# Kernel optimization log

Hardware: AMD Instinct MI355X
Metric: run time of the kernel (lower is better)

Reference implementation:

```python
import jax, jax.numpy as jnp
import numpy as np

B, S, F, H, P = 2048, 168, 7, 128, 96  # batch, window, features, hidden, pred_len


def setup_inputs() -> dict:
    key = jax.random.key(0)
    ks = jax.random.split(key, 16)
    sc = 0.05
    return {
        "xb": jax.random.normal(ks[0], (B, S, F), dtype=jnp.float32),
        # encoder LSTM (1 layer, unidirectional); gate order i,f,g,o like torch
        "W_ih_enc": jax.random.normal(ks[1], (4 * H, F), dtype=jnp.float32) * sc,
        "W_hh_enc": jax.random.normal(ks[2], (4 * H, H), dtype=jnp.float32) * sc,
        "b_ih_enc": jax.random.normal(ks[3], (4 * H,), dtype=jnp.float32) * sc,
        "b_hh_enc": jax.random.normal(ks[4], (4 * H,), dtype=jnp.float32) * sc,
        # attention linear: (H+F) -> S
        "W_att": jax.random.normal(ks[5], (S, H + F), dtype=jnp.float32) * sc,
        "b_att": jax.random.normal(ks[6], (S,), dtype=jnp.float32) * sc,
        # decoder LSTMCell: input_size=H, hidden=H
        "W_ih_dec": jax.random.normal(ks[7], (4 * H, H), dtype=jnp.float32) * sc,
        "W_hh_dec": jax.random.normal(ks[8], (4 * H, H), dtype=jnp.float32) * sc,
        "b_ih_dec": jax.random.normal(ks[9], (4 * H,), dtype=jnp.float32) * sc,
        "b_hh_dec": jax.random.normal(ks[10], (4 * H,), dtype=jnp.float32) * sc,
        # out linear: H -> F
        "W_out": jax.random.normal(ks[11], (F, H), dtype=jnp.float32) * sc,
        "b_out": jax.random.normal(ks[12], (F,), dtype=jnp.float32) * sc,
        # final linear (output_size==1 branch): F -> 1
        "W_fin": jax.random.normal(ks[13], (1, F), dtype=jnp.float32) * sc,
        "b_fin": jax.random.normal(ks[14], (1,), dtype=jnp.float32) * sc,
    }


def _gates(pre):
    i, f, g, o = jnp.split(pre, 4, axis=-1)
    return jax.nn.sigmoid(i), jax.nn.sigmoid(f), jnp.tanh(g), jax.nn.sigmoid(o)


def _forward(xb, W_ih_enc, W_hh_enc, b_ih_enc, b_hh_enc, W_att, b_att,
             W_ih_dec, W_hh_dec, b_ih_dec, b_hh_dec, W_out, b_out, W_fin, b_fin):
    b_enc = b_ih_enc + b_hh_enc
    x_ih = jnp.einsum('bsf,gf->sbg', xb, W_ih_enc)  # precompute input projections [S,B,4H]

    def enc_step(carry, xg):
        h, c = carry
        i, f, g, o = _gates(xg + h @ W_hh_enc.T + b_enc)
        c = f * c + i * g
        h = o * jnp.tanh(c)
        return (h, c), h

    h0 = jnp.zeros((xb.shape[0], W_hh_enc.shape[1]), dtype=xb.dtype)
    (h_T, _), enc_hs = jax.lax.scan(enc_step, (h0, h0), x_ih)
    encoder_output = jnp.transpose(enc_hs, (1, 0, 2))  # [B,S,H]

    b_dec = b_ih_dec + b_hh_dec

    def dec_step(carry, _):
        prev_h, y_prev = carry
        attn_in = jnp.concatenate([prev_h, y_prev], axis=1)          # [B,H+F]
        attn_w = jax.nn.softmax(attn_in @ W_att.T + b_att, axis=-1)  # [B,S]
        combine = jnp.einsum('bs,bsh->bh', attn_w, encoder_output)   # [B,H]
        # torch code: rnn_hidden, rnn_hidden = cell(combine, (prev_h, prev_h))
        # -> the CELL state c' is what survives; h'/output gate discarded.
        i, f, g, _ = _gates(combine @ W_ih_dec.T + prev_h @ W_hh_dec.T + b_dec)
        c_new = f * prev_h + i * g
        out = c_new @ W_out.T + b_out                                # [B,F]
        return (c_new, out), out

    y0 = xb[:, -1, :]
    _, outs = jax.lax.scan(dec_step, (h_T, y0), None, length=P)      # [P,B,F]
    outputs = jnp.transpose(outs, (1, 0, 2))                         # [B,P,F]
    return outputs @ W_fin.T + b_fin                                 # [B,P,1]


def reference(xb, W_ih_enc, W_hh_enc, b_ih_enc, b_hh_enc, W_att, b_att,
              W_ih_dec, W_hh_dec, b_ih_dec, b_hh_dec, W_out, b_out, W_fin, b_fin):
    return _forward(xb, W_ih_enc, W_hh_enc, b_ih_enc, b_hh_enc, W_att, b_att,
                    W_ih_dec, W_hh_dec, b_ih_dec, b_hh_dec, W_out, b_out, W_fin, b_fin)
```

## Files before the change

kernel.cpp:

```cpp
#include <hip/hip_runtime.h>
#include <hip/hip_fp8.h>

#define NB   2048
#define SEQ  168
#define NF   7
#define NH   128
#define NP   96
#define EROWS 8
#define DROWS 8
#define NTHR 512
#define KE   160
#define KD   256
#define HXS  168
#define CTS  264
#define LS4  30

typedef _Float16 h16;
typedef _Float16 h16x8 __attribute__((ext_vector_type(8)));
typedef float    f32x2 __attribute__((ext_vector_type(2)));
typedef float    f32x4 __attribute__((ext_vector_type(4)));
typedef unsigned int u32x4 __attribute__((ext_vector_type(4)));

__device__ __forceinline__ void mfma_av(f32x4& acc, h16x8 a, const h16x8& b_agpr) {
  asm("v_mfma_f32_16x16x32_f16 %0, %1, %2, %0"
      : "+v"(acc) : "v"(a), "a"(b_agpr));
}
#define PIN_A(x) asm volatile("" : "+a"(x))

__device__ __forceinline__ float sigm(float x) { return 1.f / (1.f + __expf(-x)); }
__device__ __forceinline__ float tanh_(float x) {
  float e = __expf(-2.f * fabsf(x));
  return copysignf((1.f - e) / (1.f + e), x);
}

template <bool HI>
__device__ __forceinline__ unsigned int pack2_fp8(float a, float b, unsigned int old) {
#if __has_builtin(__builtin_amdgcn_cvt_pk_fp8_f32)
  return (unsigned int)__builtin_amdgcn_cvt_pk_fp8_f32(a, b, (int)old, HI);
#else
  __hip_fp8_e4m3 qa(a), qb(b);
  unsigned int pair = (unsigned int)(*(unsigned char*)&qa) |
                      ((unsigned int)(*(unsigned char*)&qb) << 8);
  return HI ? ((old & 0x0000ffffu) | (pair << 16)) : ((old & 0xffff0000u) | pair);
#endif
}
template <bool HI>
__device__ __forceinline__ f32x2 unp2(unsigned int w) {
#if __has_builtin(__builtin_amdgcn_cvt_pk_f32_fp8)
  return __builtin_amdgcn_cvt_pk_f32_fp8(w, HI);
#else
  __hip_fp8_e4m3 a, b;
  constexpr unsigned int sh = HI ? 16 : 0;
  *(unsigned char*)&a = (w >> sh) & 0xff;
  *(unsigned char*)&b = (w >> (sh + 8)) & 0xff;
  f32x2 r; r.x = (float)a; r.y = (float)b; return r;
#endif
}

constexpr size_t WENC_OFF   = 0;
constexpr size_t WDEC_OFF   = 163840;
constexpr size_t WEFF_OFF   = 425984;
constexpr size_t BEFF_OFF   = 468992;
constexpr size_t WCOMB_OFF  = 469760;
constexpr size_t BCONST_OFF = 470272;
constexpr size_t BENC_OFF   = 470528;
constexpr size_t BDEC_OFF   = 472576;
constexpr size_t ENC2_OFF   = 31981568;
constexpr size_t HT_OFF     = 44564480;

constexpr int HIST_OFF   = 0;
constexpr int CATH_OFF   = 122880;
constexpr int ATTW_OFF   = 131328;
constexpr int WAT2_OFF   = 136704;
constexpr int D0_OFF     = 146944;
constexpr int OUTP_OFF   = 152320;
constexpr int YH_OFF     = 152576;
constexpr int DPART_OFF  = 152832;
constexpr int DPART2_OFF = 153088;
constexpr int OBUF_OFF   = 153216;
constexpr int DSMEM      = 153472;
constexpr int SHHX_OFF = 122880;
constexpr int X16_OFF  = 133632;

__global__ void setup_weights(const float* __restrict__ Wih_enc, const float* __restrict__ Whh_enc,
                              const float* __restrict__ Wih_dec, const float* __restrict__ Whh_dec,
                              const float* __restrict__ Watt, const float* __restrict__ batt,
                              const float* __restrict__ Wout, const float* __restrict__ bout,
                              const float* __restrict__ Wfin, const float* __restrict__ bfin,
                              const float* __restrict__ bihe, const float* __restrict__ bhhe,
                              const float* __restrict__ bihd, const float* __restrict__ bhhd,
                              char* __restrict__ ws) {
  int idx = blockIdx.x * blockDim.x + threadIdx.x;
  constexpr int A0 = 81920;
  constexpr int A1 = A0 + 131072;
  constexpr int A2 = A1 + 21504;
  constexpr int A3 = A2 + 168;
  constexpr int A4 = A3 + 128;
  constexpr int A5 = A4 + 1;
  constexpr int A6 = A5 + 512;
  if (idx < A0) {
    int n = idx / KE, k = idx % KE;
    float v = 0.f;
    if (k < NF) v = Wih_enc[n * NF + k];
    else if (k >= 8 && k < 136) v = Whh_enc[n * NH + (k - 8)];
    ((h16*)(ws + WENC_OFF))[idx] = (h16)v;
  } else if (idx < A1) {
    int i = idx - A0;
    int n = i / KD, k = i % KD;
    float v = (k < NH) ? Wih_dec[n * NH + k] : Whh_dec[n * NH + (k - NH)];
    ((h16*)(ws + WDEC_OFF))[i] = (h16)v;
  } else if (idx < A2) {
    int i = idx - A1;
    int s = i / NH, k = i % NH;
    float v = Watt[s * (NH + NF) + k];
    #pragma unroll
    for (int f = 0; f < NF; ++f)
      v += Watt[s * (NH + NF) + NH + f] * Wout[f * NH + k];
    ((h16*)(ws + WEFF_OFF))[i] = (h16)v;
  } else if (idx < A3) {
    int s = idx - A2;
    float v = batt[s];
    #pragma unroll
    for (int f = 0; f < NF; ++f)
      v += Watt[s * (NH + NF) + NH + f] * bout[f];
    ((float*)(ws + BEFF_OFF))[s] = v;
  } else if (idx < A4) {
    int k = idx - A3;
    float v = 0.f;
    #pragma unroll
    for (int f = 0; f < NF; ++f) v += Wfin[f] * Wout[f * NH + k];
    ((float*)(ws + WCOMB_OFF))[k] = v;
  } else if (idx < A5) {
    float v = bfin[0];
    #pragma unroll
    for (int f = 0; f < NF; ++f) v += bout[f] * Wfin[f];
    ((float*)(ws + BCONST_OFF))[0] = v;
  } else if (idx < A6) {
    int g = idx - A5;
    ((float*)(ws + BENC_OFF))[g] = bihe[g] + bhhe[g];
    ((float*)(ws + BDEC_OFF))[g] = bihd[g] + bhhd[g];
  }
}

__global__ __attribute__((amdgpu_flat_work_group_size(NTHR, NTHR), amdgpu_waves_per_eu(2, 2)))
void fused_kernel(const float* __restrict__ xb, const h16* __restrict__ w16enc,
                  const float* __restrict__ bencp, unsigned int* __restrict__ encw2,
                  float* __restrict__ hTg,
                  const float* __restrict__ Watt, const float* __restrict__ Wout,
                  const float* __restrict__ bout,
                  const h16* __restrict__ w16dec, const h16* __restrict__ weff,
                  const float* __restrict__ beffp, const float* __restrict__ wcombp,
                  const float* __restrict__ bconstp, const float* __restrict__ bdecp,
                  float* __restrict__ out) {
  extern __shared__ char smem[];
  unsigned int* hist = (unsigned int*)(smem + HIST_OFF);
  h16 (*sh_hx)[16][HXS] = (h16(*)[16][HXS])(smem + SHHX_OFF);
  h16*   x16      = (h16*)(smem + X16_OFF);
  h16*   sh_cath  = (h16*)(smem + CATH_OFF);
  float* sh_attw  = (float*)(smem + ATTW_OFF);
  h16*   sh_watt2 = (h16*)(smem + WAT2_OFF);
  float* sh_d0    = (float*)(smem + D0_OFF);
  float* sh_outp  = (float*)(smem + OUTP_OFF);
  float* sh_yh    = (float*)(smem + YH_OFF);
  float* sh_dp    = (float*)(smem + DPART_OFF);
  float* sh_dp2   = (float*)(smem + DPART2_OFF);
  float* sh_obuf  = (float*)(smem + OBUF_OFF);

  const int t  = threadIdx.x;
  const int r0 = blockIdx.x * EROWS;

  const int w  = t >> 6;
  const int l  = t & 63;
  const int lq = l >> 4;
  const int ln = l & 15;
  const int hcol = w * 16 + ln;
  const int mrow = lq * 4;
  const bool act = (lq < 2);

  for (int i = t; i < 2 * 16 * HXS; i += NTHR) ((h16*)sh_hx)[i] = (h16)0.f;
  for (int i = t; i < EROWS * SEQ * NF; i += NTHR)
    x16[i] = (h16)xb[(size_t)r0 * SEQ * NF + i];

  h16x8 bfE[4][5];
  float bE[4];
  #pragma unroll
  for (int g = 0; g < 4; ++g) {
    int n = g * 128 + hcol;
    bE[g] = bencp[n];
    #pragma unroll
    for (int kt = 0; kt < 5; ++kt) {
      bfE[g][kt] = *(const h16x8*)(w16enc + n * KE + kt * 32 + lq * 8);
      PIN_A(bfE[g][kt]);
    }
  }
  __syncthreads();
  if (t < EROWS * NF) {
    int r = t / NF, f = t - (t / NF) * NF;
    sh_hx[0][r][f] = x16[(r * SEQ + 0) * NF + f];
  }

  float creg[4] = {0.f, 0.f, 0.f, 0.f};
  float hstate[4] = {0.f, 0.f, 0.f, 0.f};
  float hprev[4] = {0.f, 0.f, 0.f, 0.f};
  unsigned int hpack[4] = {0u, 0u, 0u, 0u};

  __syncthreads();

  for (int s = 0; s < SEQ; ++s) {
    const int cur = s & 1;

    f32x4 ac[4] = {{0.f,0.f,0.f,0.f},{0.f,0.f,0.f,0.f},{0.f,0.f,0.f,0.f},{0.f,0.f,0.f,0.f}};
    #pragma unroll
    for (int kt = 0; kt < 5; ++kt) {
      h16x8 af = *(const h16x8*)(&sh_hx[cur][ln][kt * 32 + lq * 8]);
      #pragma unroll
      for (int g = 0; g < 4; ++g)
        mfma_av(ac[g], af, bfE[g][kt]);
    }

    if (act) {
      #pragma unroll
      for (int reg = 0; reg < 4; ++reg) {
        float gi = sigm(ac[0][reg] + bE[0]);
        float gf = sigm(ac[1][reg] + bE[1]);
        float gg = tanh_(ac[2][reg] + bE[2]);
        float go = sigm(ac[3][reg] + bE[3]);
        float c = gf * creg[reg] + gi * gg;
        creg[reg] = c;
        float h = go * tanh_(c);
        hstate[reg] = h;
        sh_hx[cur ^ 1][mrow + reg][8 + hcol] = (h16)h;
        float hs = h * 16.f;
        if ((s & 1) == 0) hprev[reg] = hs;
        else if ((s & 3) == 1) hpack[reg] = pack2_fp8<false>(hprev[reg], hs, hpack[reg]);
        else                   hpack[reg] = pack2_fp8<true>(hprev[reg], hs, hpack[reg]);
      }
      if ((s & 3) == 3) {
        int s4 = s >> 2;
        if (s4 < LS4) {
          #pragma unroll
          for (int reg = 0; reg < 4; ++reg)
            hist[(size_t)(mrow + reg) * (LS4 * NH) + s4 * NH + hcol] = hpack[reg];
        } else {
          int q = s4 - LS4;
          #pragma unroll
          for (int reg = 0; reg < 4; ++reg)
            encw2[(((size_t)(r0 + mrow + reg) * 3 + (q >> 2)) * NH + hcol) * 4 + (q & 3)] = hpack[reg];
        }
      }
    }
    if (t < EROWS * NF && s + 1 < SEQ) {
      int r = t / NF, f = t - (t / NF) * NF;
      sh_hx[cur ^ 1][r][f] = x16[(r * SEQ + (s + 1)) * NF + f];
    }
    __syncthreads();
  }

  if (act) {
    #pragma unroll
    for (int reg = 0; reg < 4; ++reg)
      hTg[(size_t)(r0 + mrow + reg) * NH + hcol] = hstate[reg];
  }
  __builtin_amdgcn_sched_barrier(0);
  __syncthreads();

  for (int i = t; i < 40 * NH; i += NTHR) sh_watt2[i] = weff[128 * NH + i];
  if (t < 32) sh_dp2[t] = 0.f;

  h16x8 bfD[3][8];
  float bD[3];
  #pragma unroll
  for (int g = 0; g < 3; ++g) {
    int n = g * 128 + hcol;
    bD[g] = bdecp[n];
    #pragma unroll
    for (int kt = 0; kt < 8; ++kt) {
      bfD[g][kt] = *(const h16x8*)(w16dec + n * KD + kt * 32 + lq * 8);
      PIN_A(bfD[g][kt]);
    }
  }
  h16x8 bfA[4];
  #pragma unroll
  for (int kt = 0; kt < 4; ++kt) {
    bfA[kt] = *(const h16x8*)(weff + hcol * NH + kt * 32 + lq * 8);
    PIN_A(bfA[kt]);
  }
  const float beffR = beffp[hcol];
  const int s2v = 128 + hcol;
  const float beff2 = (w < 3 && s2v < SEQ) ? beffp[s2v] : 0.f;
  const float wcombR = wcombp[hcol];
  const float bconstv = bconstp[0];

  if (act) {
    #pragma unroll
    for (int reg = 0; reg < 4; ++reg) {
      creg[reg] = hstate[reg];
      sh_cath[0 * 8 * CTS + (mrow + reg) * CTS + 128 + hcol] = (h16)hstate[reg];
    }
  }
  if (t < DROWS * NF) {
    int r = t / NF, f = t - (t / NF) * NF;
    float a = bout[f];
    const float* wr = Wout + f * NH;
    const float* hp = hTg + (size_t)(r0 + r) * NH;
    #pragma unroll 8
    for (int k = 0; k < NH; k += 4) {
      float4 pv = *(const float4*)(hp + k);
      float4 wv = *(const float4*)(wr + k);
      a += pv.x * wv.x + pv.y * wv.y + pv.z * wv.z + pv.w * wv.w;
    }
    sh_yh[t] = a;
  }
  __syncthreads();
  for (int i = t; i < DROWS * SEQ; i += NTHR) {
    int r = i / SEQ, s = i - (i / SEQ) * SEQ;
    float a = 0.f;
    #pragma unroll
    for (int f = 0; f < NF; ++f) {
      float y0f = xb[((size_t)(r0 + r) * SEQ + (SEQ - 1)) * NF + f];
      a += (y0f - sh_yh[r * NF + f]) * Watt[s * (NH + NF) + NH + f];
    }
    sh_d0[i] = a;
  }

  const int dr = t >> 7;
  const int dh = t & 127;
  const unsigned int* hrowA = hist + (size_t)dr * (LS4 * NH) + dh;
  const unsigned int* hrowB = hist + (size_t)(dr + 4) * (LS4 * NH) + dh;
  const float* erowA = sh_attw + dr * SEQ;
  const float* erowB = sh_attw + (dr + 4) * SEQ;

  u32x4 tA[3], tB[3];
  {
    const u32x4* e2 = (const u32x4*)encw2;
    #pragma unroll
    for (int b = 0; b < 3; ++b) {
      tA[b] = e2[((size_t)(r0 + dr)     * 3 + b) * NH + dh];
      tB[b] = e2[((size_t)(r0 + dr + 4) * 3 + b) * NH + dh];
    }
  }
  __syncthreads();

  f32x4 aghh[3];

  for (int p = 0; p < NP; ++p) {
    const int CA = p & 1;

    if (p > 0 && t < DROWS) {
      float a = bconstv;
      #pragma unroll
      for (int w2 = 0; w2 < 8; ++w2) a += sh_outp[w2 * 8 + t];
      int slot = (p - 1) & 7;
      sh_obuf[t * 8 + slot] = a;
      if (slot == 7) {
        int base = p - 8;
        #pragma unroll
        for (int j = 0; j < 8; ++j)
          out[(size_t)(r0 + t) * NP + base + j] = sh_obuf[t * 8 + j];
      }
    }

    {
      h16x8 afA[4];
      #pragma unroll
      for (int kt = 0; kt < 4; ++kt)
        afA[kt] = *(const h16x8*)(sh_cath + CA * 8 * CTS + (ln & 7) * CTS + 128 + kt * 32 + lq * 8);
      f32x4 acc = {0.f, 0.f, 0.f, 0.f};
      #pragma unroll
      for (int kt = 0; kt < 4; ++kt)
        mfma_av(acc, afA[kt], bfA[kt]);
      #pragma unroll
      for (int g = 0; g < 3; ++g) {
        f32x4 z = {0.f, 0.f, 0.f, 0.f};
        aghh[g] = z;
        #pragma unroll
        for (int kt = 0; kt < 4; ++kt)
          mfma_av(aghh[g], afA[kt], bfD[g][4 + kt]);
      }

      float ev[4];
      if (act) {
        #pragma unroll
        for (int reg = 0; reg < 4; ++reg) {
          int row = mrow + reg;
          float lg = acc[reg] + beffR;
          if (p == 0) lg += sh_d0[row * SEQ + hcol];
          lg = fminf(fmaxf(lg, -30.f), 30.f);
          ev[reg] = __expf(lg);
          sh_attw[row * SEQ + hcol] = ev[reg];
        }
        #pragma unroll
        for (int reg = 0; reg < 4; ++reg) {
          float rs = ev[reg];
          rs += __shfl_xor(rs, 1);
          rs += __shfl_xor(rs, 2);
          rs += __shfl_xor(rs, 4);
          rs += __shfl_xor(rs, 8);
          if (ln == 0) sh_dp[(mrow + reg) * 8 + w] = rs;
        }
      }
      if (w < 3) {
        int srow = (s2v < SEQ ? s2v : SEQ - 1) - 128;
        f32x4 acc2 = {0.f, 0.f, 0.f, 0.f};
        #pragma unroll
        for (int kt = 0; kt < 4; ++kt) {
          h16x8 bf2 = *(const h16x8*)(sh_watt2 + srow * NH + kt * 32 + lq * 8);
          acc2 = __builtin_amdgcn_mfma_f32_16x16x32_f16(afA[kt], bf2, acc2, 0, 0, 0);
        }
        if (act) {
          float ev2[4];
          #pragma unroll
          for (int reg = 0; reg < 4; ++reg) {
            int row = mrow + reg;
            float e2v = 0.f;
            if (s2v < SEQ) {
              float lg = acc2[reg] + beff2;
              if (p == 0) lg += sh_d0[row * SEQ + s2v];
              lg = fminf(fmaxf(lg, -30.f), 30.f);
              e2v = __expf(lg);
              sh_attw[row * SEQ + s2v] = e2v;
            }
            ev2[reg] = e2v;
          }
          #pragma unroll
          for (int reg = 0; reg < 4; ++reg) {
            float rs = ev2[reg];
            rs += __shfl_xor(rs, 1);
            rs += __shfl_xor(rs, 2);
            rs += __shfl_xor(rs, 4);
            rs += __shfl_xor(rs, 8);
            if (ln == 0) sh_dp2[(mrow + reg) * 4 + w] = rs;
          }
        }
      }
    }
    __syncthreads();

    {
      float4 qa0 = *(const float4*)(sh_dp + dr * 8);
      float4 qa1 = *(const float4*)(sh_dp + dr * 8 + 4);
      float4 qa2 = *(const float4*)(sh_dp2 + dr * 4);
      float4 qb0 = *(const float4*)(sh_dp + (dr + 4) * 8);
      float4 qb1 = *(const float4*)(sh_dp + (dr + 4) * 8 + 4);
      float4 qb2 = *(const float4*)(sh_dp2 + (dr + 4) * 4);
      float dA = ((qa0.x + qa0.y) + (qa0.z + qa0.w)) + ((qa1.x + qa1.y) + (qa1.z + qa1.w))
               + ((qa2.x + qa2.y) + (qa2.z + qa2.w));
      float dB = ((qb0.x + qb0.y) + (qb0.z + qb0.w)) + ((qb1.x + qb1.y) + (qb1.z + qb1.w))
               + ((qb2.x + qb2.y) + (qb2.z + qb2.w));
      const float invA = 0.0625f / dA;
      const float invB = 0.0625f / dB;

      f32x2 avA = {0.f, 0.f};
      f32x2 avB = {0.f, 0.f};
      #pragma unroll 6
      for (int s4 = 0; s4 < LS4; ++s4) {
        unsigned int evA = hrowA[s4 * NH];
        unsigned int evB = hrowB[s4 * NH];
        float4 eA = *(const float4*)(erowA + s4 * 4);
        float4 eB = *(const float4*)(erowB + s4 * 4);
        f32x2 wA01 = {eA.x, eA.y}, wA23 = {eA.z, eA.w};
        f32x2 wB01 = {eB.x, eB.y}, wB23 = {eB.z, eB.w};
        avA = wA01 * unp2<false>(evA) + avA;
        avA = wA23 * unp2<true>(evA) + avA;
        avB = wB01 * unp2<false>(evB) + avB;
        avB = wB23 * unp2<true>(evB) + avB;
      }
      #pragma unroll
      for (int b = 0; b < 3; ++b) {
        #pragma unroll
        for (int jj = 0; jj < 4; ++jj) {
          int s4 = LS4 + b * 4 + jj;
          unsigned int evA = tA[b][jj];
          unsigned int evB = tB[b][jj];
          float4 eA = *(const float4*)(erowA + s4 * 4);
          float4 eB = *(const float4*)(erowB + s4 * 4);
          f32x2 wA01 = {eA.x, eA.y}, wA23 = {eA.z, eA.w};
          f32x2 wB01 = {eB.x, eB.y}, wB23 = {eB.z, eB.w};
          avA = wA01 * unp2<false>(evA) + avA;
          avA = wA23 * unp2<true>(evA) + avA;
          avB = wB01 * unp2<false>(evB) + avB;
          avB = wB23 * unp2<true>(evB) + avB;
        }
      }
      sh_cath[CA * 8 * CTS + dr * CTS + dh]       = (h16)((avA.x + avA.y) * invA);
      sh_cath[CA * 8 * CTS + (dr + 4) * CTS + dh] = (h16)((avB.x + avB.y) * invB);
    }
    __syncthreads();

    {
      f32x4 ag[3] = {aghh[0], aghh[1], aghh[2]};
      #pragma unroll
      for (int kt = 0; kt < 4; ++kt) {
        h16x8 af = *(const h16x8*)(sh_cath + CA * 8 * CTS + (ln & 7) * CTS + kt * 32 + lq * 8);
        #pragma unroll
        for (int g = 0; g < 3; ++g)
          mfma_av(ag[g], af, bfD[g][kt]);
      }
      if (act) {
        float contrib[4];
        #pragma unroll
        for (int reg = 0; reg < 4; ++reg) {
          int row = mrow + reg;
          float gi = sigm(ag[0][reg] + bD[0]);
          float gf = sigm(ag[1][reg] + bD[1]);
          float gg = tanh_(ag[2][reg] + bD[2]);
          float cn = gf * creg[reg] + gi * gg;
          creg[reg] = cn;
          sh_cath[(CA ^ 1) * 8 * CTS + row * CTS + 128 + hcol] = (h16)cn;
          contrib[reg] = cn * wcombR;
        }
        #pragma unroll
        for (int reg = 0; reg < 4; ++reg) {
          float rsum = contrib[reg];
          rsum += __shfl_xor(rsum, 1);
          rsum += __shfl_xor(rsum, 2);
          rsum += __shfl_xor(rsum, 4);
          rsum += __shfl_xor(rsum, 8);
          if (ln == 0) sh_outp[w * 8 + mrow + reg] = rsum;
        }
      }
    }
    __syncthreads();
  }

  if (t < DROWS) {
    float a = bconstv;
    #pragma unroll
    for (int w2 = 0; w2 < 8; ++w2) a += sh_outp[w2 * 8 + t];
    sh_obuf[t * 8 + 7] = a;
    #pragma unroll
    for (int j = 0; j < 8; ++j)
      out[(size_t)(r0 + t) * NP + (NP - 8) + j] = sh_obuf[t * 8 + j];
  }
}

extern "C" void kernel_launch(void* const* d_in, const int* in_sizes, int n_in,
                              void* d_out, int out_size, void* d_ws, size_t ws_size,
                              hipStream_t stream) {
  const float* xb      = (const float*)d_in[0];
  const float* Wih_enc = (const float*)d_in[1];
  const float* Whh_enc = (const float*)d_in[2];
  const float* bih_enc = (const float*)d_in[3];
  const float* bhh_enc = (const float*)d_in[4];
  const float* Watt    = (const float*)d_in[5];
  const float* batt    = (const float*)d_in[6];
  const float* Wih_dec = (const float*)d_in[7];
  const float* Whh_dec = (const float*)d_in[8];
  const float* bih_dec = (const float*)d_in[9];
  const float* bhh_dec = (const float*)d_in[10];
  const float* Wout    = (const float*)d_in[11];
  const float* bout    = (const float*)d_in[12];
  const float* Wfin    = (const float*)d_in[13];
  const float* bfin    = (const float*)d_in[14];
  char* ws = (char*)d_ws;

  hipFuncSetAttribute(reinterpret_cast<const void*>(fused_kernel),
                      hipFuncAttributeMaxDynamicSharedMemorySize, DSMEM);

  setup_weights<<<920, 256, 0, stream>>>(Wih_enc, Whh_enc, Wih_dec, Whh_dec,
                                         Watt, batt, Wout, bout, Wfin, bfin,
                                         bih_enc, bhh_enc, bih_dec, bhh_dec, ws);
  fused_kernel<<<NB / EROWS, NTHR, DSMEM, stream>>>(
      xb, (const h16*)(ws + WENC_OFF), (const float*)(ws + BENC_OFF),
      (unsigned int*)(ws + ENC2_OFF), (float*)(ws + HT_OFF),
      Watt, Wout, bout,
      (const h16*)(ws + WDEC_OFF), (const h16*)(ws + WEFF_OFF),
      (const float*)(ws + BEFF_OFF), (const float*)(ws + WCOMB_OFF),
      (const float*)(ws + BCONST_OFF), (const float*)(ws + BDEC_OFF),
      (float*)d_out);
}
```

Baseline: 996.0 us.

## Stream encoder inputs from global, recompute softmax denominators, drop early hidden MFMAs

The encoder no longer stages the whole x window in LDS. Each group of threads prefetches four future timesteps into a register every fourth step and writes them into the shared input tile. In the decoder, the softmax denominator is now recomputed by a full-wave shuffle reduction over the stored exponentials instead of per-warp partial sums kept in shared memory. The hidden-state gate MFMAs are moved back into the post-attention gate loop (8 k-tiles instead of 4), which shortens the attention phase but lengthens the gate phase and adds global loads inside the recurrent loop.

```diff
diff --git a/kernel.cpp b/kernel.cpp
--- a/kernel.cpp
+++ b/kernel.cpp
@@ -75,12 +75,9 @@
 constexpr int D0_OFF     = 146944;
 constexpr int OUTP_OFF   = 152320;
 constexpr int YH_OFF     = 152576;
-constexpr int DPART_OFF  = 152832;
-constexpr int DPART2_OFF = 153088;
-constexpr int OBUF_OFF   = 153216;
-constexpr int DSMEM      = 153472;
+constexpr int OBUF_OFF   = 152832;
+constexpr int DSMEM      = 153088;
 constexpr int SHHX_OFF = 122880;
-constexpr int X16_OFF  = 133632;
 
 __global__ void setup_weights(const float* __restrict__ Wih_enc, const float* __restrict__ Whh_enc,
                               const float* __restrict__ Wih_dec, const float* __restrict__ Whh_dec,
@@ -155,15 +152,12 @@
   extern __shared__ char smem[];
   unsigned int* hist = (unsigned int*)(smem + HIST_OFF);
   h16 (*sh_hx)[16][HXS] = (h16(*)[16][HXS])(smem + SHHX_OFF);
-  h16*   x16      = (h16*)(smem + X16_OFF);
   h16*   sh_cath  = (h16*)(smem + CATH_OFF);
   float* sh_attw  = (float*)(smem + ATTW_OFF);
   h16*   sh_watt2 = (h16*)(smem + WAT2_OFF);
   float* sh_d0    = (float*)(smem + D0_OFF);
   float* sh_outp  = (float*)(smem + OUTP_OFF);
   float* sh_yh    = (float*)(smem + YH_OFF);
-  float* sh_dp    = (float*)(smem + DPART_OFF);
-  float* sh_dp2   = (float*)(smem + DPART2_OFF);
   float* sh_obuf  = (float*)(smem + OBUF_OFF);
 
   const int t  = threadIdx.x;
@@ -177,9 +171,12 @@
   const int mrow = lq * 4;
   const bool act = (lq < 2);
 
+  const int j  = t & 3;
+  const int rf = t >> 2;
+  const int xr = rf / NF;
+  const int xf = rf - xr * NF;
+
   for (int i = t; i < 2 * 16 * HXS; i += NTHR) ((h16*)sh_hx)[i] = (h16)0.f;
-  for (int i = t; i < EROWS * SEQ * NF; i += NTHR)
-    x16[i] = (h16)xb[(size_t)r0 * SEQ * NF + i];
 
   h16x8 bfE[4][5];
   float bE[4];
@@ -196,18 +193,23 @@
   __syncthreads();
   if (t < EROWS * NF) {
     int r = t / NF, f = t - (t / NF) * NF;
-    sh_hx[0][r][f] = x16[(r * SEQ + 0) * NF + f];
+    sh_hx[0][r][f] = (h16)xb[((size_t)(r0 + r) * SEQ + 0) * NF + f];
   }
 
   float creg[4] = {0.f, 0.f, 0.f, 0.f};
   float hstate[4] = {0.f, 0.f, 0.f, 0.f};
   float hprev[4] = {0.f, 0.f, 0.f, 0.f};
   unsigned int hpack[4] = {0u, 0u, 0u, 0u};
+  float xstash = 0.f;
 
   __syncthreads();
 
   for (int s = 0; s < SEQ; ++s) {
     const int cur = s & 1;
+    if ((s & 3) == 0 && t < EROWS * NF * 4) {
+      int sx = s + 1 + j;
+      xstash = (sx < SEQ) ? xb[((size_t)(r0 + xr) * SEQ + sx) * NF + xf] : 0.f;
+    }
 
     f32x4 ac[4] = {{0.f,0.f,0.f,0.f},{0.f,0.f,0.f,0.f},{0.f,0.f,0.f,0.f},{0.f,0.f,0.f,0.f}};
     #pragma unroll
@@ -249,10 +251,8 @@
         }
       }
     }
-    if (t < EROWS * NF && s + 1 < SEQ) {
-      int r = t / NF, f = t - (t / NF) * NF;
-      sh_hx[cur ^ 1][r][f] = x16[(r * SEQ + (s + 1)) * NF + f];
-    }
+    if (t < EROWS * NF * 4 && (s & 3) == j && s + 1 < SEQ)
+      sh_hx[cur ^ 1][xr][xf] = (h16)xstash;
     __syncthreads();
   }
 
@@ -261,11 +261,9 @@
     for (int reg = 0; reg < 4; ++reg)
       hTg[(size_t)(r0 + mrow + reg) * NH + hcol] = hstate[reg];
   }
-  __builtin_amdgcn_sched_barrier(0);
   __syncthreads();
 
   for (int i = t; i < 40 * NH; i += NTHR) sh_watt2[i] = weff[128 * NH + i];
-  if (t < 32) sh_dp2[t] = 0.f;
 
   h16x8 bfD[3][8];
   float bD[3];
@@ -341,8 +339,6 @@
   }
   __syncthreads();
 
-  f32x4 aghh[3];
-
   for (int p = 0; p < NP; ++p) {
     const int CA = p & 1;
 
@@ -355,8 +351,8 @@
       if (slot == 7) {
         int base = p - 8;
         #pragma unroll
-        for (int j = 0; j < 8; ++j)
-          out[(size_t)(r0 + t) * NP + base + j] = sh_obuf[t * 8 + j];
+        for (int jj = 0; jj < 8; ++jj)
+          out[(size_t)(r0 + t) * NP + base + jj] = sh_obuf[t * 8 + jj];
       }
     }
 
@@ -369,16 +365,6 @@
       #pragma unroll
       for (int kt = 0; kt < 4; ++kt)
         mfma_av(acc, afA[kt], bfA[kt]);
-      #pragma unroll
-      for (int g = 0; g < 3; ++g) {
-        f32x4 z = {0.f, 0.f, 0.f, 0.f};
-        aghh[g] = z;
-        #pragma unroll
-        for (int kt = 0; kt < 4; ++kt)
-          mfma_av(aghh[g], afA[kt], bfD[g][4 + kt]);
-      }
-
-      float ev[4];
       if (act) {
         #pragma unroll
         for (int reg = 0; reg < 4; ++reg) {
@@ -386,17 +372,7 @@
           float lg = acc[reg] + beffR;
           if (p == 0) lg += sh_d0[row * SEQ + hcol];
           lg = fminf(fmaxf(lg, -30.f), 30.f);
-          ev[reg] = __expf(lg);
-          sh_attw[row * SEQ + hcol] = ev[reg];
-        }
-        #pragma unroll
-        for (int reg = 0; reg < 4; ++reg) {
-          float rs = ev[reg];
-          rs += __shfl_xor(rs, 1);
-          rs += __shfl_xor(rs, 2);
-          rs += __shfl_xor(rs, 4);
-          rs += __shfl_xor(rs, 8);
-          if (ln == 0) sh_dp[(mrow + reg) * 8 + w] = rs;
+          sh_attw[row * SEQ + hcol] = __expf(lg);
         }
       }
       if (w < 3) {
@@ -407,46 +383,29 @@
           h16x8 bf2 = *(const h16x8*)(sh_watt2 + srow * NH + kt * 32 + lq * 8);
           acc2 = __builtin_amdgcn_mfma_f32_16x16x32_f16(afA[kt], bf2, acc2, 0, 0, 0);
         }
-        if (act) {
-          float ev2[4];
+        if (s2v < SEQ && act) {
           #pragma unroll
           for (int reg = 0; reg < 4; ++reg) {
             int row = mrow + reg;
-            float e2v = 0.f;
-            if (s2v < SEQ) {
-              float lg = acc2[reg] + beff2;
-              if (p == 0) lg += sh_d0[row * SEQ + s2v];
-              lg = fminf(fmaxf(lg, -30.f), 30.f);
-              e2v = __expf(lg);
-              sh_attw[row * SEQ + s2v] = e2v;
-            }
-            ev2[reg] = e2v;
+            float lg = acc2[reg] + beff2;
+            if (p == 0) lg += sh_d0[row * SEQ + s2v];
+            lg = fminf(fmaxf(lg, -30.f), 30.f);
+            sh_attw[row * SEQ + s2v] = __expf(lg);
           }
-          #pragma unroll
-          for (int reg = 0; reg < 4; ++reg) {
-            float rs = ev2[reg];
-            rs += __shfl_xor(rs, 1);
-            rs += __shfl_xor(rs, 2);
-            rs += __shfl_xor(rs, 4);
-            rs += __shfl_xor(rs, 8);
-            if (ln == 0) sh_dp2[(mrow + reg) * 4 + w] = rs;
-          }
         }
       }
     }
     __syncthreads();
 
     {
-      float4 qa0 = *(const float4*)(sh_dp + dr * 8);
-      float4 qa1 = *(const float4*)(sh_dp + dr * 8 + 4);
-      float4 qa2 = *(const float4*)(sh_dp2 + dr * 4);
-      float4 qb0 = *(const float4*)(sh_dp + (dr + 4) * 8);
-      float4 qb1 = *(const float4*)(sh_dp + (dr + 4) * 8 + 4);
-      float4 qb2 = *(const float4*)(sh_dp2 + (dr + 4) * 4);
-      float dA = ((qa0.x + qa0.y) + (qa0.z + qa0.w)) + ((qa1.x + qa1.y) + (qa1.z + qa1.w))
-               + ((qa2.x + qa2.y) + (qa2.z + qa2.w));
-      float dB = ((qb0.x + qb0.y) + (qb0.z + qb0.w)) + ((qb1.x + qb1.y) + (qb1.z + qb1.w))
-               + ((qb2.x + qb2.y) + (qb2.z + qb2.w));
+      float dA = erowA[l] + erowA[64 + l];
+      float dB = erowB[l] + erowB[64 + l];
+      if (l < SEQ - 128) { dA += erowA[128 + l]; dB += erowB[128 + l]; }
+      #pragma unroll
+      for (int k = 1; k < 64; k <<= 1) {
+        dA += __shfl_xor(dA, k);
+        dB += __shfl_xor(dB, k);
+      }
       const float invA = 0.0625f / dA;
       const float invB = 0.0625f / dB;
 
@@ -488,9 +447,9 @@
     __syncthreads();
 
     {
-      f32x4 ag[3] = {aghh[0], aghh[1], aghh[2]};
-      #pragma unroll
-      for (int kt = 0; kt < 4; ++kt) {
+      f32x4 ag[3] = {{0.f,0.f,0.f,0.f},{0.f,0.f,0.f,0.f},{0.f,0.f,0.f,0.f}};
+      #pragma unroll
+      for (int kt = 0; kt < 8; ++kt) {
         h16x8 af = *(const h16x8*)(sh_cath + CA * 8 * CTS + (ln & 7) * CTS + kt * 32 + lq * 8);
         #pragma unroll
         for (int g = 0; g < 3; ++g)
@@ -529,8 +488,8 @@
     for (int w2 = 0; w2 < 8; ++w2) a += sh_outp[w2 * 8 + t];
     sh_obuf[t * 8 + 7] = a;
     #pragma unroll
-    for (int j = 0; j < 8; ++j)
-      out[(size_t)(r0 + t) * NP + (NP - 8) + j] = sh_obuf[t * 8 + j];
+    for (int jj = 0; jj < 8; ++jj)
+      out[(size_t)(r0 + t) * NP + (NP - 8) + jj] = sh_obuf[t * 8 + jj];
   }
 }
 
```

New measurement: 905.5 us. 9.1% less time.
